# Kernel tuning notes

Measured on AMD Instinct MI355X. Metric: run time of the kernel, lower is better.

The kernel has to match this reference:

```python
import jax, jax.numpy as jnp
import numpy as np


def _lstm_cell(x, h, c, Wih, Whh, b):
    # torch LSTM gate order: i, f, g, o
    g = x @ Wih.T + h @ Whh.T + b
    i, f, gg, o = jnp.split(g, 4, axis=-1)
    c = jax.nn.sigmoid(f) * c + jax.nn.sigmoid(i) * jnp.tanh(gg)
    h = jax.nn.sigmoid(o) * jnp.tanh(c)
    return h, c


def _run_lstm(emb, mask, Wih, Whh, b, reverse):
    # mask-gated scan emulates pack_padded_sequence: state frozen on pad steps,
    # final (h, c) equals state at last valid token of each sequence.
    B = emb.shape[0]
    H = Whh.shape[1]
    def step(carry, inp):
        h, c = carry
        x, m = inp  # x: (B, E), m: (B, 1)
        hn, cn = _lstm_cell(x, h, c, Wih, Whh, b)
        h = m * hn + (1.0 - m) * h
        c = m * cn + (1.0 - m) * c
        return (h, c), h
    xs = (jnp.swapaxes(emb, 0, 1), jnp.swapaxes(mask, 0, 1)[..., None])
    z = jnp.zeros((B, H), emb.dtype)
    (h, c), outs = jax.lax.scan(step, (z, z), xs, reverse=reverse)
    return jnp.swapaxes(outs, 0, 1), h, c  # (B, T, H), (B, H), (B, H)


def setup_inputs() -> dict:
    key = jax.random.key(0)
    ks = iter(jax.random.split(key, 40))
    B, Te, Td, E, H, Ve, Vd = 32, 64, 32, 256, 512, 32000, 32000
    s = 0.05
    def rn(shape):
        return jax.random.normal(next(ks), shape, jnp.float32) * s
    def zz(n):
        return jnp.zeros((n,), jnp.float32)
    return {
        "enc_texts": jax.random.randint(next(ks), (B, Te), 0, Ve),
        "enc_mask": jnp.ones((B, Te), jnp.float32),
        "dec_texts": jax.random.randint(next(ks), (B, Td), 0, Vd),
        "enc_emb": rn((Ve, E)),
        "dec_emb": rn((Vd, E)),
        "Wih_f": rn((4 * H, E)), "Whh_f": rn((4 * H, H)), "b_f": zz(4 * H),
        "Wih_b": rn((4 * H, E)), "Whh_b": rn((4 * H, H)), "b_b": zz(4 * H),
        "Wih_d": rn((4 * H, E + 2 * H)), "Whh_d": rn((4 * H, H)), "b_d": zz(4 * H),
        "W_h": rn((H, 2 * H)), "b_h": zz(H),
        "W_c": rn((H, 2 * H)), "b_c": zz(H),
        "W_df": rn((2 * H, 2 * H)), "b_df": zz(2 * H),
        "W_ef": rn((2 * H, 2 * H)), "b_ef": zz(2 * H),
        "W_out": rn((Vd, 3 * H)), "b_out": zz(Vd),
    }


def reference(enc_texts, enc_mask, dec_texts, enc_emb, dec_emb,
              Wih_f, Whh_f, b_f, Wih_b, Whh_b, b_b,
              Wih_d, Whh_d, b_d, W_h, b_h, W_c, b_c,
              W_df, b_df, W_ef, b_ef, W_out, b_out):
    B = enc_texts.shape[0]
    H = Whh_d.shape[1]
    # ---- encode: bidirectional LSTM over embedded source ----
    emb = enc_emb[enc_texts]  # (B, Te, E)
    out_f, hf, cf = _run_lstm(emb, enc_mask, Wih_f, Whh_f, b_f, reverse=False)
    out_b, hb, cb = _run_lstm(emb, enc_mask, Wih_b, Whh_b, b_b, reverse=True)
    enc_output = jnp.concatenate([out_f, out_b], -1) * enc_mask[..., None]  # (B, Te, 2H)
    # ---- decode_init: project concat of directional final states ----
    dec_h = jax.nn.relu(jnp.concatenate([hf, hb], -1) @ W_h.T + b_h)  # (B, H)
    dec_c = jax.nn.relu(jnp.concatenate([cf, cb], -1) @ W_c.T + b_c)  # (B, H)
    # precompute attention keys once (enc_output_fc)
    enc_feat = enc_output @ W_ef.T + b_ef  # (B, Te, 2H)
    # teacher-forcing inputs: tokens 0..Td-2
    dec_in = dec_emb[dec_texts[:, :-1]]  # (B, Td-1, E)
    ctx0 = jnp.zeros((B, 2 * H), enc_output.dtype)

    def step(carry, x):
        h, c, ctx = carry
        xin = jnp.concatenate([x, ctx], -1)  # (B, E + 2H)
        h, c = _lstm_cell(xin, h, c, Wih_d, Whh_d, b_d)
        # dot attention: query from projected (h, c)
        df = jnp.concatenate([h, c], -1) @ W_df.T + b_df  # (B, 2H)
        scores = jnp.einsum('bd,btd->bt', df, enc_feat)
        a = jax.nn.softmax(scores, axis=-1) * enc_mask
        a = a / jnp.sum(a, axis=-1, keepdims=True)
        ctx = jnp.einsum('bt,btd->bd', a, enc_output)  # (B, 2H)
        logits = jnp.concatenate([h, ctx], -1) @ W_out.T + b_out  # (B, Vd)
        return (h, c, ctx), logits

    _, logits = jax.lax.scan(step, (dec_h, dec_c, ctx0), jnp.swapaxes(dec_in, 0, 1))
    return jnp.swapaxes(logits, 0, 1)  # (B, Td-1, Vd)
```

## Files before the change

kernel.cpp:

```cpp
#include <hip/hip_runtime.h>
#include <hip/hip_bf16.h>


typedef __attribute__((ext_vector_type(8))) short bfrag_t;
typedef __attribute__((ext_vector_type(4))) float f4_t;

static __device__ __forceinline__ float bf2f(unsigned short u) {
  union { float f; unsigned int i; } v; v.i = ((unsigned int)u) << 16; return v.f;
}
static __device__ __forceinline__ unsigned short f2bf(float f) {
  union { float f; unsigned int i; } v; v.f = f;
  unsigned int r = v.i + 0x7FFFu + ((v.i >> 16) & 1u);
  return (unsigned short)(r >> 16);
}
static __device__ __forceinline__ unsigned int pack_bf2(float lo, float hi) {
  __hip_bfloat162 h2 = __float22bfloat162_rn(make_float2(lo, hi));
  union { __hip_bfloat162 h; unsigned int u; } cv; cv.h = h2;
  return cv.u;
}
static __device__ __forceinline__ float sigm(float x) {
  return __builtin_amdgcn_rcpf(1.f + __expf(-x));
}
static __device__ __forceinline__ float ftanh(float x) {
  float e = __expf(2.f * x);
  return 1.f - 2.f * __builtin_amdgcn_rcpf(e + 1.f);
}

#define GLDS16(g, l)                                                        \
  __builtin_amdgcn_global_load_lds(                                         \
      (const __attribute__((address_space(1))) void*)(g),                   \
      (__attribute__((address_space(3))) void*)(l), 16, 0, 0)

static __device__ __forceinline__ void st_f32_coh(float* p, float v) {
  asm volatile("global_store_dword %0, %1, off sc0 sc1" :: "v"(p), "v"(v) : "memory");
}
static __device__ __forceinline__ void st_u16_coh(unsigned short* p, unsigned short x) {
  asm volatile("global_store_short %0, %1, off sc0 sc1" :: "v"(p), "v"((unsigned)x) : "memory");
}
static __device__ __forceinline__ float ld_f32_coh(const float* p) {
  float v;
  asm volatile("global_load_dword %0, %1, off sc0 sc1\n\ts_waitcnt vmcnt(0)"
               : "=v"(v) : "v"(p) : "memory");
  return v;
}

static __device__ __forceinline__ void arrive8(unsigned* base) {
  __syncthreads();
  if (threadIdx.x == 0)
    __hip_atomic_fetch_add(base + (blockIdx.x & 7) * 32, 1u,
                           __ATOMIC_RELAXED, __HIP_MEMORY_SCOPE_AGENT);
}
static __device__ __forceinline__ void wait8(unsigned* base, unsigned target) {
  if (threadIdx.x < 64) {
    unsigned sum;
    do {
      unsigned v = 0;
      if (threadIdx.x < 8)
        v = __hip_atomic_load(base + threadIdx.x * 32,
                              __ATOMIC_RELAXED, __HIP_MEMORY_SCOPE_AGENT);
      v += __shfl_xor(v, 1);
      v += __shfl_xor(v, 2);
      v += __shfl_xor(v, 4);
      sum = __shfl(v, 0);
      if (sum < target) __builtin_amdgcn_s_sleep(2);
    } while (sum < target);
  }
  __syncthreads();
}
static __device__ __forceinline__ void gbar8(unsigned* base, unsigned target) {
  arrive8(base);
  wait8(base, target);
}

__global__ __launch_bounds__(256) void gemm_bt_kernel(
    const unsigned short* __restrict__ A, int lda,
    const float* __restrict__ B, int ldb, int bcol0,
    const float* __restrict__ bias, void* __restrict__ Cv, int ldc,
    int Mvalid, int K, int Mt, int swz, int obf) {
  __shared__ unsigned short As[128 * 32];
  __shared__ unsigned short Bs[128 * 32];
  int id = blockIdx.x;
  if (swz) { int x = id & 7; id = x * ((int)gridDim.x >> 3) + (id >> 3); }
  const int mb = id % Mt, nb = id / Mt;
  const int m0 = mb * 128, n0 = nb * 128;
  const int tid = threadIdx.x;
  const int w = tid >> 6, lane = tid & 63;
  const int wr = (w >> 1) * 64, wc = (w & 1) * 64;
  const int l15 = lane & 15, l4 = lane >> 4;

  const int arow = w * 16 + (lane >> 2);
  const int acol = (lane & 3) * 8;
  const unsigned short* Ag = A + (size_t)(m0 + arow) * lda + acol;

  const int brow = tid >> 1;
  const int bcol = (tid & 1) * 16;
  const float* Bg = B + (size_t)(n0 + brow) * ldb + bcol0 + bcol;
  unsigned short* Bsw = Bs + brow * 32 + bcol;

  f4_t acc[4][4];
#pragma unroll
  for (int i = 0; i < 4; ++i)
#pragma unroll
    for (int j = 0; j < 4; ++j) {
      acc[i][j].x = 0.f; acc[i][j].y = 0.f; acc[i][j].z = 0.f; acc[i][j].w = 0.f;
    }

  for (int kt = 0; kt < K; kt += 32) {
    GLDS16(Ag + kt, As + w * 512);
    GLDS16(Ag + (size_t)64 * lda + kt, As + (4 + w) * 512);
    float4 q0 = *(const float4*)(Bg + kt);
    float4 q1 = *(const float4*)(Bg + kt + 4);
    float4 q2 = *(const float4*)(Bg + kt + 8);
    float4 q3 = *(const float4*)(Bg + kt + 12);
    union { unsigned int u[8]; uint4 q[2]; } pk;
    pk.u[0] = pack_bf2(q0.x, q0.y); pk.u[1] = pack_bf2(q0.z, q0.w);
    pk.u[2] = pack_bf2(q1.x, q1.y); pk.u[3] = pack_bf2(q1.z, q1.w);
    pk.u[4] = pack_bf2(q2.x, q2.y); pk.u[5] = pack_bf2(q2.z, q2.w);
    pk.u[6] = pack_bf2(q3.x, q3.y); pk.u[7] = pack_bf2(q3.z, q3.w);
    *(uint4*)(Bsw) = pk.q[0];
    *(uint4*)(Bsw + 8) = pk.q[1];
    __syncthreads();
    bfrag_t af[4], bfv[4];
#pragma unroll
    for (int m = 0; m < 4; ++m)
      af[m] = *(const bfrag_t*)(As + (wr + m * 16 + l15) * 32 + l4 * 8);
#pragma unroll
    for (int n = 0; n < 4; ++n)
      bfv[n] = *(const bfrag_t*)(Bs + (wc + n * 16 + l15) * 32 + l4 * 8);
#pragma unroll
    for (int m = 0; m < 4; ++m)
#pragma unroll
      for (int n = 0; n < 4; ++n)
        acc[m][n] = __builtin_amdgcn_mfma_f32_16x16x32_bf16(af[m], bfv[n], acc[m][n], 0, 0, 0);
    __syncthreads();
  }

  const int crb = l4 * 4;
  float* Cf = (float*)Cv;
  unsigned short* Ch = (unsigned short*)Cv;
#pragma unroll
  for (int m = 0; m < 4; ++m)
#pragma unroll
    for (int n = 0; n < 4; ++n)
#pragma unroll
      for (int r = 0; r < 4; ++r) {
        int gr = m0 + wr + m * 16 + crb + r;
        if (gr < Mvalid) {
          int gc = n0 + wc + n * 16 + l15;
          float v = acc[m][n][r] + (bias ? bias[gc] : 0.f);
          if (obf) Ch[(size_t)gr * ldc + gc] = f2bf(v);
          else     Cf[(size_t)gr * ldc + gc] = v;
        }
      }
}

__global__ __launch_bounds__(256) void gemm_bt16_kernel(
    const unsigned short* __restrict__ A, int lda,
    const unsigned short* __restrict__ B, int ldb,
    const float* __restrict__ bias, float* __restrict__ C, int ldc,
    int Mvalid, int K, int Mt, int swz) {
  __shared__ unsigned short As[128 * 32];
  __shared__ unsigned short Bs[128 * 32];
  int id = blockIdx.x;
  if (swz) { int x = id & 7; id = x * ((int)gridDim.x >> 3) + (id >> 3); }
  const int mb = id % Mt, nb = id / Mt;
  const int m0 = mb * 128, n0 = nb * 128;
  const int tid = threadIdx.x;
  const int w = tid >> 6, lane = tid & 63;
  const int wr = (w >> 1) * 64, wc = (w & 1) * 64;
  const int l15 = lane & 15, l4 = lane >> 4;

  const int arow = w * 16 + (lane >> 2);
  const int acol = (lane & 3) * 8;
  const unsigned short* Ag = A + (size_t)(m0 + arow) * lda + acol;
  const unsigned short* Bg = B + (size_t)(n0 + arow) * ldb + acol;

  f4_t acc[4][4];
#pragma unroll
  for (int i = 0; i < 4; ++i)
#pragma unroll
    for (int j = 0; j < 4; ++j) {
      acc[i][j].x = 0.f; acc[i][j].y = 0.f; acc[i][j].z = 0.f; acc[i][j].w = 0.f;
    }

  for (int kt = 0; kt < K; kt += 32) {
    GLDS16(Ag + kt, As + w * 512);
    GLDS16(Ag + (size_t)64 * lda + kt, As + (4 + w) * 512);
    GLDS16(Bg + kt, Bs + w * 512);
    GLDS16(Bg + (size_t)64 * ldb + kt, Bs + (4 + w) * 512);
    __syncthreads();
    bfrag_t af[4], bfv[4];
#pragma unroll
    for (int m = 0; m < 4; ++m)
      af[m] = *(const bfrag_t*)(As + (wr + m * 16 + l15) * 32 + l4 * 8);
#pragma unroll
    for (int n = 0; n < 4; ++n)
      bfv[n] = *(const bfrag_t*)(Bs + (wc + n * 16 + l15) * 32 + l4 * 8);
#pragma unroll
    for (int m = 0; m < 4; ++m)
#pragma unroll
      for (int n = 0; n < 4; ++n)
        acc[m][n] = __builtin_amdgcn_mfma_f32_16x16x32_bf16(af[m], bfv[n], acc[m][n], 0, 0, 0);
    __syncthreads();
  }

  const int crb = l4 * 4;
#pragma unroll
  for (int m = 0; m < 4; ++m)
#pragma unroll
    for (int n = 0; n < 4; ++n)
#pragma unroll
      for (int r = 0; r < 4; ++r) {
        int gr = m0 + wr + m * 16 + crb + r;
        if (gr < Mvalid) {
          int gc = n0 + wc + n * 16 + l15;
          C[(size_t)gr * ldc + gc] = acc[m][n][r] + bias[gc];
        }
      }
}

__global__ __launch_bounds__(256) void wout_bf16_kernel(
    const float* __restrict__ src, unsigned short* __restrict__ dst) {
  size_t base = (size_t)blockIdx.x * 2048 + threadIdx.x * 8;
  float4 a = *(const float4*)(src + base);
  float4 b = *(const float4*)(src + base + 4);
  uint4 o;
  o.x = pack_bf2(a.x, a.y); o.y = pack_bf2(a.z, a.w);
  o.z = pack_bf2(b.x, b.y); o.w = pack_bf2(b.z, b.w);
  *(uint4*)(dst + base) = o;
}

__global__ void gather_enc_kernel(const int* __restrict__ texts,
                                  const float* __restrict__ table,
                                  unsigned short* __restrict__ out) {
  const int row = blockIdx.x;
  const int tok = texts[row];
  const float4 v = *(const float4*)(table + (size_t)tok * 256 + threadIdx.x * 4);
  unsigned short* o = out + (size_t)row * 256 + threadIdx.x * 4;
  o[0] = f2bf(v.x); o[1] = f2bf(v.y); o[2] = f2bf(v.z); o[3] = f2bf(v.w);
}

__global__ void gather_dec_kernel(const int* __restrict__ texts,
                                  const float* __restrict__ table,
                                  unsigned short* __restrict__ out) {
  const int row = blockIdx.x;
  unsigned short* o = out + (size_t)row * 256 + threadIdx.x * 4;
  if (row >= 992) { o[0] = 0; o[1] = 0; o[2] = 0; o[3] = 0; return; }
  const int b = row / 31, t2 = row - b * 31;
  const int tok = texts[b * 32 + t2];
  const float4 v = *(const float4*)(table + (size_t)tok * 256 + threadIdx.x * 4);
  o[0] = f2bf(v.x); o[1] = f2bf(v.y); o[2] = f2bf(v.z); o[3] = f2bf(v.w);
}

__global__ __launch_bounds__(256) void wdf_t_kernel(
    const float* __restrict__ W_df, const float* __restrict__ b_df,
    float* __restrict__ WT) {
  const int bid = blockIdx.x;
  if (bid < 1024) {
    __shared__ float tl[32][33];
    const int tx = (bid & 31) * 32, ty = (bid >> 5) * 32;
    const int r = threadIdx.x >> 5, c = threadIdx.x & 31;
#pragma unroll
    for (int i = 0; i < 4; ++i)
      tl[r + i * 8][c] = W_df[(size_t)(ty + r + i * 8) * 1024 + tx + c];
    __syncthreads();
#pragma unroll
    for (int i = 0; i < 4; ++i)
      WT[(size_t)(tx + r + i * 8) * 1024 + ty + c] = tl[c][r + i * 8];
  } else {
    for (int i = threadIdx.x; i < 1024; i += 256)
      WT[(size_t)1024 * 1024 + i] = b_df[i];
  }
}

__global__ __launch_bounds__(256) void mega_enc_kernel(
    const float* __restrict__ XF, const float* __restrict__ XB,
    const float* __restrict__ Whh_f, const float* __restrict__ Whh_b,
    const float* __restrict__ mask,
    unsigned short* __restrict__ HBF,
    unsigned short* __restrict__ ENCO, float* __restrict__ HFIN,
    unsigned* bar) {
  const int bi = blockIdx.x;
  const int dir = bi >> 6;
  const int u0 = (bi & 63) * 8;
  const int tid = threadIdx.x;
  const float* X = dir ? XB : XF;
  const float* W = dir ? Whh_b : Whh_f;
  unsigned short* Hbf = HBF + dir * 32768;
  unsigned* cnt = bar + dir * 256;

  __shared__ unsigned short WA[32 * 520];
  __shared__ unsigned short HB[32 * 520];
  __shared__ float Gl[32][33];

#pragma unroll
  for (int i = 0; i < 16; ++i) {
    int idx = tid + i * 256;
    int r = idx >> 7, c4 = idx & 127;
    const float4 v = *(const float4*)(W + (size_t)((r >> 3) * 512 + u0 + (r & 7)) * 512 + c4 * 4);
    *(uint2*)(WA + r * 520 + c4 * 4) = make_uint2(pack_bf2(v.x, v.y), pack_bf2(v.z, v.w));
  }
  __syncthreads();

  const int w = tid >> 6, lane = tid & 63;
  const int l15 = lane & 15, l4 = lane >> 4;
  const int wrow = (w >> 1) * 16, wcol = (w & 1) * 16;

  bfrag_t afr[16];
#pragma unroll
  for (int kk = 0; kk < 16; ++kk)
    afr[kk] = *(const bfrag_t*)(WA + (wrow + l15) * 520 + kk * 32 + l4 * 8);

  const int ob = tid & 31, ouo = tid >> 5;
  const int ou = u0 + ouo;
  float h_reg = 0.f, c_reg = 0.f;

  unsigned tgt = 0;
  for (int s = 0; s < 64; ++s) {
    const int t = dir ? (63 - s) : s;
    const int pp = s & 1;
    const float* xp = X + ((size_t)ob * 64 + t) * 2048 + ou;
    float xg0 = xp[0], xg1 = xp[512], xg2 = xp[1024], xg3 = xp[1536];
    float mval = mask[ob * 64 + t];
    const unsigned short* hsrc = Hbf + pp * 16384;
    uint4 tmp[8];
#pragma unroll
    for (int i = 0; i < 8; ++i) {
      int idx = tid + i * 256;
      int r = idx >> 6, c = idx & 63;
      asm volatile("global_load_dwordx4 %0, %1, off sc0 sc1"
                   : "=v"(tmp[i]) : "v"(hsrc + r * 512 + c * 8));
    }
    asm volatile("s_waitcnt vmcnt(0)" ::: "memory");
#pragma unroll
    for (int i = 0; i < 8; ++i) {
      int idx = tid + i * 256;
      int r = idx >> 6, c = idx & 63;
      *(uint4*)(HB + r * 520 + c * 8) = tmp[i];
    }
    __syncthreads();
    {
      f4_t ae = {0.f, 0.f, 0.f, 0.f}, ao = {0.f, 0.f, 0.f, 0.f};
#pragma unroll
      for (int kk = 0; kk < 16; kk += 2) {
        bfrag_t b0 = *(const bfrag_t*)(HB + (wcol + l15) * 520 + kk * 32 + l4 * 8);
        bfrag_t b1 = *(const bfrag_t*)(HB + (wcol + l15) * 520 + (kk + 1) * 32 + l4 * 8);
        ae = __builtin_amdgcn_mfma_f32_16x16x32_bf16(afr[kk], b0, ae, 0, 0, 0);
        ao = __builtin_amdgcn_mfma_f32_16x16x32_bf16(afr[kk + 1], b1, ao, 0, 0, 0);
      }
#pragma unroll
      for (int r = 0; r < 4; ++r)
        Gl[wrow + l4 * 4 + r][wcol + l15] = ae[r] + ao[r];
    }
    __syncthreads();
    {
      float gi = Gl[ouo][ob] + xg0;
      float gf = Gl[8 + ouo][ob] + xg1;
      float gg = Gl[16 + ouo][ob] + xg2;
      float go = Gl[24 + ouo][ob] + xg3;
      float cn = sigm(gf) * c_reg + sigm(gi) * ftanh(gg);
      float hn = sigm(go) * ftanh(cn);
      float hmix = mval * hn + (1.f - mval) * h_reg;
      float cmix = mval * cn + (1.f - mval) * c_reg;
      h_reg = hmix; c_reg = cmix;
      ENCO[((size_t)ob * 64 + t) * 1024 + dir * 512 + ou] = f2bf(hmix * mval);
      st_u16_coh(Hbf + (pp ^ 1) * 16384 + ob * 512 + ou, f2bf(hmix));
      if (s == 63) {
        HFIN[dir * 16384 + ob * 512 + ou] = hmix;
        HFIN[(2 + dir) * 16384 + ob * 512 + ou] = cmix;
      }
    }
    if (s < 63) { tgt += 64; gbar8(cnt, tgt); }
  }
}

__global__ __launch_bounds__(256) void mega_dec_kernel(
    const float* __restrict__ HFIN, const float* __restrict__ W_h,
    const float* __restrict__ b_h, const float* __restrict__ W_c,
    const float* __restrict__ b_c, const float* __restrict__ XD,
    const float* __restrict__ Wih_d, const float* __restrict__ Whh_d,
    const unsigned short* __restrict__ EFG, const unsigned short* __restrict__ ENCO,
    const float* __restrict__ mask, float* __restrict__ DECH,
    float* __restrict__ DECC, unsigned short* __restrict__ PRE0,
    unsigned short* __restrict__ ACAT, unsigned* bar) {
  const int bi = blockIdx.x;
  const int tid = threadIdx.x;
  const bool is_attn = (bi >= 128);
  const int u0 = bi * 4;
  unsigned* barB1 = bar;
  unsigned* barB2 = bar + 256;

  __shared__ union {
    struct {
      unsigned short wga[16 * 1544];
      unsigned short xb[32 * 1544];
      float gl[16][33];
    } s;
    struct {
      unsigned short efg[64 * 1160];
      float hcl[1024];
      float scl[64];
      float al[64];
    } a;
    struct { float xl[32][132]; float wi[8][132]; } ini;
  } U;

  const int ob = tid & 31, ouo = (tid >> 5) & 3, ou = u0 + ouo;
  const int w = tid >> 6, lane = tid & 63;
  const int l15 = lane & 15, l4 = lane >> 4;

  if (!is_attn) {
    {
      const int mat = bi >> 6, j0i = (bi & 63) * 8;
      const int jj = tid >> 5, b = tid & 31;
      const int sr = tid >> 5, sc = (tid & 31) * 4;
      const float* Wm = mat ? W_c : W_h;
      const float* bias = mat ? b_c : b_h;
      const float* x0 = HFIN + (size_t)(mat ? 2 : 0) * 16384;
      const float* x1 = HFIN + (size_t)(mat ? 3 : 1) * 16384;
      float acc = 0.f;
      for (int kc = 0; kc < 1024; kc += 128) {
#pragma unroll
        for (int i = 0; i < 4; ++i) {
          int r = sr + i * 8;
          const float* src = (kc < 512) ? (x0 + r * 512 + kc + sc)
                                        : (x1 + r * 512 + (kc - 512) + sc);
          *(float4*)&U.ini.xl[r][sc] = *(const float4*)src;
        }
        *(float4*)&U.ini.wi[sr][sc] = *(const float4*)(Wm + (size_t)(j0i + sr) * 1024 + kc + sc);
        __syncthreads();
#pragma unroll
        for (int k = 0; k < 128; k += 4) {
          float4 wv = *(const float4*)&U.ini.wi[jj][k];
          float4 xv = *(const float4*)&U.ini.xl[b][k];
          acc += wv.x * xv.x + wv.y * xv.y + wv.z * xv.z + wv.w * xv.w;
        }
        __syncthreads();
      }
      float v = fmaxf(acc + bias[j0i + jj], 0.f);
      if (mat == 0) {
        st_f32_coh(DECH + b * 512 + j0i + jj, v);
        st_u16_coh(PRE0 + (size_t)b * 1536 + j0i + jj, f2bf(v));
      } else {
        st_f32_coh(DECC + b * 512 + j0i + jj, v);
      }
    }
    arrive8(barB1);
    wait8(barB1, 128);

#pragma unroll
    for (int i = 0; i < 24; ++i) {
      int idx = tid + i * 256;
      int r = idx / 384, c4 = idx - (idx / 384) * 384;
      int wrow = (r >> 2) * 512 + u0 + (r & 3);
      int c = c4 * 4;
      float4 v;
      if (c < 512) v = *(const float4*)(Whh_d + (size_t)wrow * 512 + c);
      else         v = *(const float4*)(Wih_d + (size_t)wrow * 1280 + 256 + (c - 512));
      *(uint2*)(U.s.wga + r * 1544 + c) = make_uint2(pack_bf2(v.x, v.y), pack_bf2(v.z, v.w));
    }
    float h_reg = 0.f, c_reg = 0.f;
    if (tid < 128) {
      h_reg = ld_f32_coh(DECH + ob * 512 + ou);
      c_reg = ld_f32_coh(DECC + ob * 512 + ou);
    }

    f4_t cae = {0.f, 0.f, 0.f, 0.f}, cao = {0.f, 0.f, 0.f, 0.f};

    for (int t = 0; t < 31; ++t) {
      float xg0 = 0, xg1 = 0, xg2 = 0, xg3 = 0;
      if (tid < 128) {
        const float* xp = XD + ((size_t)ob * 31 + t) * 2048 + ou;
        xg0 = xp[0]; xg1 = xp[512]; xg2 = xp[1024]; xg3 = xp[1536];
      }
      if (t == 0) {
        uint4 tmp[24];
#pragma unroll
        for (int i = 0; i < 24; ++i) {
          int idx = tid + i * 256;
          int r = idx / 192, c16 = idx - (idx / 192) * 192;
          asm volatile("global_load_dwordx4 %0, %1, off sc0 sc1"
                       : "=v"(tmp[i]) : "v"(PRE0 + (size_t)r * 1536 + c16 * 8));
        }
        asm volatile("s_waitcnt vmcnt(0)" ::: "memory");
#pragma unroll
        for (int i = 0; i < 24; ++i) {
          int idx = tid + i * 256;
          int r = idx / 192, c16 = idx - (idx / 192) * 192;
          *(uint4*)(U.s.xb + r * 1544 + c16 * 8) = tmp[i];
        }
        __syncthreads();
        if (w < 2) {
          f4_t ae = {0.f, 0.f, 0.f, 0.f}, ao = {0.f, 0.f, 0.f, 0.f};
#pragma unroll
          for (int kk = 0; kk < 48; kk += 2) {
            bfrag_t a0 = *(const bfrag_t*)(U.s.wga + l15 * 1544 + kk * 32 + l4 * 8);
            bfrag_t b0 = *(const bfrag_t*)(U.s.xb + (w * 16 + l15) * 1544 + kk * 32 + l4 * 8);
            bfrag_t a1 = *(const bfrag_t*)(U.s.wga + l15 * 1544 + (kk + 1) * 32 + l4 * 8);
            bfrag_t b1 = *(const bfrag_t*)(U.s.xb + (w * 16 + l15) * 1544 + (kk + 1) * 32 + l4 * 8);
            ae = __builtin_amdgcn_mfma_f32_16x16x32_bf16(a0, b0, ae, 0, 0, 0);
            ao = __builtin_amdgcn_mfma_f32_16x16x32_bf16(a1, b1, ao, 0, 0, 0);
          }
#pragma unroll
          for (int r = 0; r < 4; ++r)
            U.s.gl[l4 * 4 + r][w * 16 + l15] = ae[r] + ao[r];
        }
      } else {
        wait8(barB2, 32u * t);
        uint4 tmp[16];
#pragma unroll
        for (int i = 0; i < 16; ++i) {
          int idx = tid + i * 256;
          int r = idx >> 7, c16 = 64 + (idx & 127);
          asm volatile("global_load_dwordx4 %0, %1, off sc0 sc1"
                       : "=v"(tmp[i]) : "v"(ACAT + ((size_t)r * 31 + (t - 1)) * 1536 + c16 * 8));
        }
        asm volatile("s_waitcnt vmcnt(8)" ::: "memory");
#pragma unroll
        for (int i = 0; i < 8; ++i) {
          int idx = tid + i * 256;
          int r = idx >> 7, c16 = 64 + (idx & 127);
          *(uint4*)(U.s.xb + r * 1544 + c16 * 8) = tmp[i];
        }
        asm volatile("s_waitcnt vmcnt(0)" ::: "memory");
#pragma unroll
        for (int i = 8; i < 16; ++i) {
          int idx = tid + i * 256;
          int r = idx >> 7, c16 = 64 + (idx & 127);
          *(uint4*)(U.s.xb + r * 1544 + c16 * 8) = tmp[i];
        }
        __syncthreads();
        if (w < 2) {
          f4_t ae = cae, ao = cao;
#pragma unroll
          for (int kk = 16; kk < 48; kk += 2) {
            bfrag_t a0 = *(const bfrag_t*)(U.s.wga + l15 * 1544 + kk * 32 + l4 * 8);
            bfrag_t b0 = *(const bfrag_t*)(U.s.xb + (w * 16 + l15) * 1544 + kk * 32 + l4 * 8);
            bfrag_t a1 = *(const bfrag_t*)(U.s.wga + l15 * 1544 + (kk + 1) * 32 + l4 * 8);
            bfrag_t b1 = *(const bfrag_t*)(U.s.xb + (w * 16 + l15) * 1544 + (kk + 1) * 32 + l4 * 8);
            ae = __builtin_amdgcn_mfma_f32_16x16x32_bf16(a0, b0, ae, 0, 0, 0);
            ao = __builtin_amdgcn_mfma_f32_16x16x32_bf16(a1, b1, ao, 0, 0, 0);
          }
#pragma unroll
          for (int r = 0; r < 4; ++r)
            U.s.gl[l4 * 4 + r][w * 16 + l15] = ae[r] + ao[r];
        }
      }
      __syncthreads();
      if (tid < 128) {
        float gi = U.s.gl[ouo][ob] + xg0;
        float gf = U.s.gl[4 + ouo][ob] + xg1;
        float gg = U.s.gl[8 + ouo][ob] + xg2;
        float go = U.s.gl[12 + ouo][ob] + xg3;
        float cn = sigm(gf) * c_reg + sigm(gi) * ftanh(gg);
        float hn = sigm(go) * ftanh(cn);
        h_reg = hn; c_reg = cn;
        st_f32_coh(DECH + ob * 512 + ou, hn);
        st_f32_coh(DECC + ob * 512 + ou, cn);
        st_u16_coh(ACAT + ((size_t)ob * 31 + t) * 1536 + ou, f2bf(hn));
      }
      arrive8(barB1);
      if (t < 30) {
        wait8(barB1, 128u * (t + 2));
        uint4 pre[8];
#pragma unroll
        for (int i = 0; i < 8; ++i) {
          int idx = tid + i * 256;
          int r = idx >> 6, c16 = idx & 63;
          asm volatile("global_load_dwordx4 %0, %1, off sc0 sc1"
                       : "=v"(pre[i]) : "v"(ACAT + ((size_t)r * 31 + t) * 1536 + c16 * 8));
        }
        asm volatile("s_waitcnt vmcnt(0)" ::: "memory");
#pragma unroll
        for (int i = 0; i < 8; ++i) {
          int idx = tid + i * 256;
          int r = idx >> 6, c16 = idx & 63;
          *(uint4*)(U.s.xb + r * 1544 + c16 * 8) = pre[i];
        }
        __syncthreads();
        if (w < 2) {
          f4_t ae = {0.f, 0.f, 0.f, 0.f}, ao = {0.f, 0.f, 0.f, 0.f};
#pragma unroll
          for (int kk = 0; kk < 16; kk += 2) {
            bfrag_t a0 = *(const bfrag_t*)(U.s.wga + l15 * 1544 + kk * 32 + l4 * 8);
            bfrag_t b0 = *(const bfrag_t*)(U.s.xb + (w * 16 + l15) * 1544 + kk * 32 + l4 * 8);
            bfrag_t a1 = *(const bfrag_t*)(U.s.wga + l15 * 1544 + (kk + 1) * 32 + l4 * 8);
            bfrag_t b1 = *(const bfrag_t*)(U.s.xb + (w * 16 + l15) * 1544 + (kk + 1) * 32 + l4 * 8);
            ae = __builtin_amdgcn_mfma_f32_16x16x32_bf16(a0, b0, ae, 0, 0, 0);
            ao = __builtin_amdgcn_mfma_f32_16x16x32_bf16(a1, b1, ao, 0, 0, 0);
          }
          cae = ae; cao = ao;
        }
      }
    }
  } else {
    const int b = bi - 128;
    for (int idx = tid; idx < 64 * 144; idx += 256) {
      int s = idx / 144, c16 = idx - (idx / 144) * 144;
      *(uint4*)(U.a.efg + s * 1160 + c16 * 8) =
          *(const uint4*)(EFG + ((size_t)b * 64 + s) * 1152 + c16 * 8);
    }
    for (int t = 0; t < 31; ++t) {
      wait8(barB1, 128u * (t + 2));
      {
        int c = tid * 4;
        const float* hp = (c < 512) ? (DECH + b * 512 + c) : (DECC + b * 512 + (c - 512));
        uint4 hv;
        asm volatile("global_load_dwordx4 %0, %1, off sc0 sc1\n\ts_waitcnt vmcnt(0)"
                     : "=v"(hv) : "v"(hp) : "memory");
        *(uint4*)&U.a.hcl[c] = hv;
      }
      __syncthreads();
      {
        const int sidx = tid >> 2, part = tid & 3;
        const unsigned short* eg = U.a.efg + sidx * 1160 + part * 256;
        const float* d = &U.a.hcl[part * 256];
        float acc = 0.f;
#pragma unroll 8
        for (int k = 0; k < 256; k += 8) {
          uint4 v = *(const uint4*)(eg + k);
          acc += bf2f((unsigned short)(v.x & 0xFFFFu)) * d[k + 0];
          acc += bf2f((unsigned short)(v.x >> 16))     * d[k + 1];
          acc += bf2f((unsigned short)(v.y & 0xFFFFu)) * d[k + 2];
          acc += bf2f((unsigned short)(v.y >> 16))     * d[k + 3];
          acc += bf2f((unsigned short)(v.z & 0xFFFFu)) * d[k + 4];
          acc += bf2f((unsigned short)(v.z >> 16))     * d[k + 5];
          acc += bf2f((unsigned short)(v.w & 0xFFFFu)) * d[k + 6];
          acc += bf2f((unsigned short)(v.w >> 16))     * d[k + 7];
        }
        acc += __shfl_xor(acc, 1);
        acc += __shfl_xor(acc, 2);
        if (part == 0)
          U.a.scl[sidx] = acc + bf2f(U.a.efg[sidx * 1160 + 1024]);
      }
      __syncthreads();
      if (tid < 64) {
        float v = U.a.scl[tid];
        float mx = v;
#pragma unroll
        for (int o = 32; o >= 1; o >>= 1) mx = fmaxf(mx, __shfl_xor(mx, o));
        float e = __expf(v - mx) * mask[b * 64 + tid];
        float sm = e;
#pragma unroll
        for (int o = 32; o >= 1; o >>= 1) sm += __shfl_xor(sm, o);
        U.a.al[tid] = e / sm;
      }
      __syncthreads();
      float c0 = 0.f, c1 = 0.f, c2 = 0.f, c3 = 0.f;
#pragma unroll 8
      for (int tp = 0; tp < 64; ++tp) {
        float a = U.a.al[tp];
        const unsigned short* eo = ENCO + ((size_t)b * 64 + tp) * 1024 + tid;
        c0 += a * bf2f(eo[0]);
        c1 += a * bf2f(eo[256]);
        c2 += a * bf2f(eo[512]);
        c3 += a * bf2f(eo[768]);
      }
      unsigned short* ap = ACAT + ((size_t)b * 31 + t) * 1536 + 512;
      st_u16_coh(ap + tid, f2bf(c0));
      st_u16_coh(ap + tid + 256, f2bf(c1));
      st_u16_coh(ap + tid + 512, f2bf(c2));
      st_u16_coh(ap + tid + 768, f2bf(c3));
      arrive8(barB2);
    }
  }
}

extern "C" void kernel_launch(void* const* d_in, const int* in_sizes, int n_in,
                              void* d_out, int out_size, void* d_ws, size_t ws_size,
                              hipStream_t stream) {
  const int*   enc_texts = (const int*)  d_in[0];
  const float* enc_mask  = (const float*)d_in[1];
  const int*   dec_texts = (const int*)  d_in[2];
  const float* enc_emb   = (const float*)d_in[3];
  const float* dec_emb   = (const float*)d_in[4];
  const float* Wih_f = (const float*)d_in[5];
  const float* Whh_f = (const float*)d_in[6];
  const float* b_f   = (const float*)d_in[7];
  const float* Wih_b = (const float*)d_in[8];
  const float* Whh_b = (const float*)d_in[9];
  const float* b_b   = (const float*)d_in[10];
  const float* Wih_d = (const float*)d_in[11];
  const float* Whh_d = (const float*)d_in[12];
  const float* b_d   = (const float*)d_in[13];
  const float* W_h   = (const float*)d_in[14];
  const float* b_h   = (const float*)d_in[15];
  const float* W_c   = (const float*)d_in[16];
  const float* b_c   = (const float*)d_in[17];
  const float* W_df  = (const float*)d_in[18];
  const float* b_df  = (const float*)d_in[19];
  const float* W_ef  = (const float*)d_in[20];
  const float* b_ef  = (const float*)d_in[21];
  const float* W_out = (const float*)d_in[22];
  const float* b_out = (const float*)d_in[23];
  float* out = (float*)d_out;

  char* ws = (char*)d_ws;
  size_t off = 0;
  auto alloc = [&](size_t bytes) {
    char* p = ws + off;
    off += (bytes + 255) & ~(size_t)255;
    return p;
  };
  unsigned short* HBF  = (unsigned short*)alloc((size_t)2 * 2 * 16384 * 2);
  float* DECH = (float*)alloc((size_t)16384 * 4);
  float* DECC = (float*)alloc((size_t)16384 * 4);
  unsigned short* PRE0 = (unsigned short*)alloc((size_t)32 * 1536 * 2);
  unsigned short* ACAT = (unsigned short*)alloc((size_t)1024 * 1536 * 2);
  unsigned* bar = (unsigned*)alloc(4096);
  unsigned* barD = bar + 512;
  size_t zbytes = off;
  float* XF = (float*)alloc((size_t)2048 * 2048 * 4);
  float* XB = (float*)alloc((size_t)2048 * 2048 * 4);
  float* XD = (float*)alloc((size_t)1024 * 2048 * 4);
  unsigned short* EFb  = (unsigned short*)alloc((size_t)2048 * 1024 * 2);
  unsigned short* ENCO = (unsigned short*)alloc((size_t)2048 * 1024 * 2);
  unsigned short* EMBB = (unsigned short*)alloc((size_t)2048 * 256 * 2);
  unsigned short* DEMB = (unsigned short*)alloc((size_t)1024 * 256 * 2);
  float* HFIN = (float*)alloc((size_t)4 * 16384 * 4);
  unsigned short* EFG = (unsigned short*)XF;
  float* WT  = XB;
  unsigned short* WOB = (unsigned short*)alloc((size_t)32000 * 1536 * 2);
  const bool use16 = (off <= ws_size);

  hipMemsetAsync(d_ws, 0, zbytes, stream);

  gather_enc_kernel<<<2048, 64, 0, stream>>>(enc_texts, enc_emb, EMBB);
  gather_dec_kernel<<<1024, 64, 0, stream>>>(dec_texts, dec_emb, DEMB);
  if (use16)
    wout_bf16_kernel<<<24000, 256, 0, stream>>>(W_out, WOB);

  dim3 blk(256);
  gemm_bt_kernel<<<256, blk, 0, stream>>>(EMBB, 256, Wih_f, 256, 0, b_f, XF, 2048, 2048, 256, 16, 0, 0);
  gemm_bt_kernel<<<256, blk, 0, stream>>>(EMBB, 256, Wih_b, 256, 0, b_b, XB, 2048, 2048, 256, 16, 0, 0);
  gemm_bt_kernel<<<128, blk, 0, stream>>>(DEMB, 256, Wih_d, 1280, 0, b_d, XD, 2048, 1024, 256, 8, 0, 0);

  mega_enc_kernel<<<128, blk, 0, stream>>>(XF, XB, Whh_f, Whh_b, enc_mask, HBF, ENCO, HFIN, bar);

  wdf_t_kernel<<<1025, blk, 0, stream>>>(W_df, b_df, WT);
  gemm_bt_kernel<<<128, blk, 0, stream>>>(ENCO, 1024, W_ef, 1024, 0, b_ef, EFb, 1024, 2048, 1024, 16, 0, 1);
  gemm_bt_kernel<<<144, blk, 0, stream>>>(EFb, 1024, WT, 1024, 0, nullptr, EFG, 1152, 2048, 1024, 16, 0, 1);

  mega_dec_kernel<<<160, blk, 0, stream>>>(HFIN, W_h, b_h, W_c, b_c, XD, Wih_d, Whh_d,
                                           EFG, ENCO, enc_mask, DECH, DECC, PRE0, ACAT, barD);

  if (use16)
    gemm_bt16_kernel<<<2000, blk, 0, stream>>>(ACAT, 1536, WOB, 1536, b_out, out, 32000, 992, 1536, 8, 1);
  else
    gemm_bt_kernel<<<2000, blk, 0, stream>>>(ACAT, 1536, W_out, 1536, 0, b_out, out, 32000, 992, 1536, 8, 1, 0);
}
```

Measured before the change: 1.237 ms.

## Overlap weight conversion and W_df transpose with recurrent LSTM kernels

The standalone W_df transpose is folded into the encoder recurrent kernel as extra idle blocks, and the W_out fp32-to-bf16 conversion is folded into the decoder kernel as 64 extra blocks. Both conversions now run on otherwise unused CUs while the latency-bound recurrences execute. The encoder recurrence is also restructured to use 64 blocks of 16 units each instead of 128 blocks of 8, so fewer blocks take part in each grid barrier. The cost is a larger per-block weight footprint and more work per block, and WT gets its own buffer because it can no longer alias XB while XB is still being read. Memory traffic from the side work may contend with the latency-sensitive recurrent steps.

```diff
diff --git a/kernel.cpp b/kernel.cpp
--- a/kernel.cpp
+++ b/kernel.cpp
@@ -219,17 +219,6 @@
       }
 }
 
-__global__ __launch_bounds__(256) void wout_bf16_kernel(
-    const float* __restrict__ src, unsigned short* __restrict__ dst) {
-  size_t base = (size_t)blockIdx.x * 2048 + threadIdx.x * 8;
-  float4 a = *(const float4*)(src + base);
-  float4 b = *(const float4*)(src + base + 4);
-  uint4 o;
-  o.x = pack_bf2(a.x, a.y); o.y = pack_bf2(a.z, a.w);
-  o.z = pack_bf2(b.x, b.y); o.w = pack_bf2(b.z, b.w);
-  *(uint4*)(dst + base) = o;
-}
-
 __global__ void gather_enc_kernel(const int* __restrict__ texts,
                                   const float* __restrict__ table,
                                   unsigned short* __restrict__ out) {
@@ -252,75 +241,87 @@
   o[0] = f2bf(v.x); o[1] = f2bf(v.y); o[2] = f2bf(v.z); o[3] = f2bf(v.w);
 }
 
-__global__ __launch_bounds__(256) void wdf_t_kernel(
-    const float* __restrict__ W_df, const float* __restrict__ b_df,
-    float* __restrict__ WT) {
-  const int bid = blockIdx.x;
-  if (bid < 1024) {
-    __shared__ float tl[32][33];
-    const int tx = (bid & 31) * 32, ty = (bid >> 5) * 32;
-    const int r = threadIdx.x >> 5, c = threadIdx.x & 31;
-#pragma unroll
-    for (int i = 0; i < 4; ++i)
-      tl[r + i * 8][c] = W_df[(size_t)(ty + r + i * 8) * 1024 + tx + c];
-    __syncthreads();
-#pragma unroll
-    for (int i = 0; i < 4; ++i)
-      WT[(size_t)(tx + r + i * 8) * 1024 + ty + c] = tl[c][r + i * 8];
-  } else {
-    for (int i = threadIdx.x; i < 1024; i += 256)
-      WT[(size_t)1024 * 1024 + i] = b_df[i];
-  }
-}
-
 __global__ __launch_bounds__(256) void mega_enc_kernel(
     const float* __restrict__ XF, const float* __restrict__ XB,
     const float* __restrict__ Whh_f, const float* __restrict__ Whh_b,
     const float* __restrict__ mask,
     unsigned short* __restrict__ HBF,
     unsigned short* __restrict__ ENCO, float* __restrict__ HFIN,
-    unsigned* bar) {
+    const float* __restrict__ W_df, const float* __restrict__ b_df,
+    float* __restrict__ WT, unsigned* bar) {
   const int bi = blockIdx.x;
-  const int dir = bi >> 6;
-  const int u0 = (bi & 63) * 8;
   const int tid = threadIdx.x;
+
+  __shared__ union {
+    struct {
+      unsigned short WA[64 * 520];
+      unsigned short HB[32 * 520];
+      float Gl[64][33];
+    } e;
+    struct { float tl[32][33]; } tr;
+  } S;
+
+  if (bi >= 64) {
+    for (int job = bi - 64; job < 1025; job += 160) {
+      if (job < 1024) {
+        const int tx = (job & 31) * 32, ty = (job >> 5) * 32;
+        const int r = tid >> 5, c = tid & 31;
+#pragma unroll
+        for (int i = 0; i < 4; ++i)
+          S.tr.tl[r + i * 8][c] = W_df[(size_t)(ty + r + i * 8) * 1024 + tx + c];
+        __syncthreads();
+#pragma unroll
+        for (int i = 0; i < 4; ++i)
+          WT[(size_t)(tx + r + i * 8) * 1024 + ty + c] = S.tr.tl[c][r + i * 8];
+        __syncthreads();
+      } else {
+        for (int i = tid; i < 1024; i += 256)
+          WT[(size_t)1024 * 1024 + i] = b_df[i];
+      }
+    }
+    return;
+  }
+
+  const int dir = bi >> 5;
+  const int u0 = (bi & 31) * 16;
   const float* X = dir ? XB : XF;
   const float* W = dir ? Whh_b : Whh_f;
   unsigned short* Hbf = HBF + dir * 32768;
   unsigned* cnt = bar + dir * 256;
 
-  __shared__ unsigned short WA[32 * 520];
-  __shared__ unsigned short HB[32 * 520];
-  __shared__ float Gl[32][33];
-
-#pragma unroll
-  for (int i = 0; i < 16; ++i) {
+#pragma unroll
+  for (int i = 0; i < 32; ++i) {
     int idx = tid + i * 256;
     int r = idx >> 7, c4 = idx & 127;
-    const float4 v = *(const float4*)(W + (size_t)((r >> 3) * 512 + u0 + (r & 7)) * 512 + c4 * 4);
-    *(uint2*)(WA + r * 520 + c4 * 4) = make_uint2(pack_bf2(v.x, v.y), pack_bf2(v.z, v.w));
+    const float4 v = *(const float4*)(W + (size_t)((r >> 4) * 512 + u0 + (r & 15)) * 512 + c4 * 4);
+    *(uint2*)(S.e.WA + r * 520 + c4 * 4) = make_uint2(pack_bf2(v.x, v.y), pack_bf2(v.z, v.w));
   }
   __syncthreads();
 
   const int w = tid >> 6, lane = tid & 63;
   const int l15 = lane & 15, l4 = lane >> 4;
-  const int wrow = (w >> 1) * 16, wcol = (w & 1) * 16;
+  const int wrow = w * 16;
 
   bfrag_t afr[16];
 #pragma unroll
   for (int kk = 0; kk < 16; ++kk)
-    afr[kk] = *(const bfrag_t*)(WA + (wrow + l15) * 520 + kk * 32 + l4 * 8);
+    afr[kk] = *(const bfrag_t*)(S.e.WA + (wrow + l15) * 520 + kk * 32 + l4 * 8);
 
   const int ob = tid & 31, ouo = tid >> 5;
-  const int ou = u0 + ouo;
-  float h_reg = 0.f, c_reg = 0.f;
+  float h_reg0 = 0.f, c_reg0 = 0.f, h_reg1 = 0.f, c_reg1 = 0.f;
 
   unsigned tgt = 0;
   for (int s = 0; s < 64; ++s) {
     const int t = dir ? (63 - s) : s;
     const int pp = s & 1;
-    const float* xp = X + ((size_t)ob * 64 + t) * 2048 + ou;
-    float xg0 = xp[0], xg1 = xp[512], xg2 = xp[1024], xg3 = xp[1536];
+    const float* xp = X + ((size_t)ob * 64 + t) * 2048 + u0;
+    float xg[2][4];
+#pragma unroll
+    for (int p = 0; p < 2; ++p) {
+      int ul = ouo + p * 8;
+      xg[p][0] = xp[ul]; xg[p][1] = xp[512 + ul];
+      xg[p][2] = xp[1024 + ul]; xg[p][3] = xp[1536 + ul];
+    }
     float mval = mask[ob * 64 + t];
     const unsigned short* hsrc = Hbf + pp * 16384;
     uint4 tmp[8];
@@ -336,28 +337,35 @@
     for (int i = 0; i < 8; ++i) {
       int idx = tid + i * 256;
       int r = idx >> 6, c = idx & 63;
-      *(uint4*)(HB + r * 520 + c * 8) = tmp[i];
+      *(uint4*)(S.e.HB + r * 520 + c * 8) = tmp[i];
     }
     __syncthreads();
     {
-      f4_t ae = {0.f, 0.f, 0.f, 0.f}, ao = {0.f, 0.f, 0.f, 0.f};
-#pragma unroll
-      for (int kk = 0; kk < 16; kk += 2) {
-        bfrag_t b0 = *(const bfrag_t*)(HB + (wcol + l15) * 520 + kk * 32 + l4 * 8);
-        bfrag_t b1 = *(const bfrag_t*)(HB + (wcol + l15) * 520 + (kk + 1) * 32 + l4 * 8);
-        ae = __builtin_amdgcn_mfma_f32_16x16x32_bf16(afr[kk], b0, ae, 0, 0, 0);
-        ao = __builtin_amdgcn_mfma_f32_16x16x32_bf16(afr[kk + 1], b1, ao, 0, 0, 0);
-      }
-#pragma unroll
-      for (int r = 0; r < 4; ++r)
-        Gl[wrow + l4 * 4 + r][wcol + l15] = ae[r] + ao[r];
+      f4_t a0 = {0.f, 0.f, 0.f, 0.f}, a1 = {0.f, 0.f, 0.f, 0.f};
+#pragma unroll
+      for (int kk = 0; kk < 16; ++kk) {
+        bfrag_t b0 = *(const bfrag_t*)(S.e.HB + l15 * 520 + kk * 32 + l4 * 8);
+        bfrag_t b1 = *(const bfrag_t*)(S.e.HB + (16 + l15) * 520 + kk * 32 + l4 * 8);
+        a0 = __builtin_amdgcn_mfma_f32_16x16x32_bf16(afr[kk], b0, a0, 0, 0, 0);
+        a1 = __builtin_amdgcn_mfma_f32_16x16x32_bf16(afr[kk], b1, a1, 0, 0, 0);
+      }
+#pragma unroll
+      for (int r = 0; r < 4; ++r) {
+        S.e.Gl[wrow + l4 * 4 + r][l15] = a0[r];
+        S.e.Gl[wrow + l4 * 4 + r][16 + l15] = a1[r];
+      }
     }
     __syncthreads();
-    {
-      float gi = Gl[ouo][ob] + xg0;
-      float gf = Gl[8 + ouo][ob] + xg1;
-      float gg = Gl[16 + ouo][ob] + xg2;
-      float go = Gl[24 + ouo][ob] + xg3;
+#pragma unroll
+    for (int p = 0; p < 2; ++p) {
+      const int ul = ouo + p * 8;
+      const int ou = u0 + ul;
+      float& h_reg = p ? h_reg1 : h_reg0;
+      float& c_reg = p ? c_reg1 : c_reg0;
+      float gi = S.e.Gl[ul][ob] + xg[p][0];
+      float gf = S.e.Gl[16 + ul][ob] + xg[p][1];
+      float gg = S.e.Gl[32 + ul][ob] + xg[p][2];
+      float go = S.e.Gl[48 + ul][ob] + xg[p][3];
       float cn = sigm(gf) * c_reg + sigm(gi) * ftanh(gg);
       float hn = sigm(go) * ftanh(cn);
       float hmix = mval * hn + (1.f - mval) * h_reg;
@@ -370,7 +378,7 @@
         HFIN[(2 + dir) * 16384 + ob * 512 + ou] = cmix;
       }
     }
-    if (s < 63) { tgt += 64; gbar8(cnt, tgt); }
+    if (s < 63) { tgt += 32; gbar8(cnt, tgt); }
   }
 }
 
@@ -382,9 +390,28 @@
     const unsigned short* __restrict__ EFG, const unsigned short* __restrict__ ENCO,
     const float* __restrict__ mask, float* __restrict__ DECH,
     float* __restrict__ DECC, unsigned short* __restrict__ PRE0,
-    unsigned short* __restrict__ ACAT, unsigned* bar) {
+    unsigned short* __restrict__ ACAT,
+    const float* __restrict__ W_out, unsigned short* __restrict__ WOB,
+    int do_conv, unsigned* bar) {
   const int bi = blockIdx.x;
   const int tid = threadIdx.x;
+
+  if (bi >= 160) {
+    if (do_conv) {
+      const int cb = bi - 160;
+      for (size_t base = (size_t)cb * 2048 + tid * 8;
+           base < (size_t)32000 * 1536; base += (size_t)64 * 2048) {
+        float4 a = *(const float4*)(W_out + base);
+        float4 b = *(const float4*)(W_out + base + 4);
+        uint4 o;
+        o.x = pack_bf2(a.x, a.y); o.y = pack_bf2(a.z, a.w);
+        o.z = pack_bf2(b.x, b.y); o.w = pack_bf2(b.z, b.w);
+        *(uint4*)(WOB + base) = o;
+      }
+    }
+    return;
+  }
+
   const bool is_attn = (bi >= 128);
   const int u0 = bi * 4;
   unsigned* barB1 = bar;
@@ -718,8 +745,8 @@
   unsigned short* EMBB = (unsigned short*)alloc((size_t)2048 * 256 * 2);
   unsigned short* DEMB = (unsigned short*)alloc((size_t)1024 * 256 * 2);
   float* HFIN = (float*)alloc((size_t)4 * 16384 * 4);
+  float* WT = (float*)alloc((size_t)1152 * 1024 * 4);
   unsigned short* EFG = (unsigned short*)XF;
-  float* WT  = XB;
   unsigned short* WOB = (unsigned short*)alloc((size_t)32000 * 1536 * 2);
   const bool use16 = (off <= ws_size);
 
@@ -727,22 +754,21 @@
 
   gather_enc_kernel<<<2048, 64, 0, stream>>>(enc_texts, enc_emb, EMBB);
   gather_dec_kernel<<<1024, 64, 0, stream>>>(dec_texts, dec_emb, DEMB);
-  if (use16)
-    wout_bf16_kernel<<<24000, 256, 0, stream>>>(W_out, WOB);
 
   dim3 blk(256);
   gemm_bt_kernel<<<256, blk, 0, stream>>>(EMBB, 256, Wih_f, 256, 0, b_f, XF, 2048, 2048, 256, 16, 0, 0);
   gemm_bt_kernel<<<256, blk, 0, stream>>>(EMBB, 256, Wih_b, 256, 0, b_b, XB, 2048, 2048, 256, 16, 0, 0);
   gemm_bt_kernel<<<128, blk, 0, stream>>>(DEMB, 256, Wih_d, 1280, 0, b_d, XD, 2048, 1024, 256, 8, 0, 0);
 
-  mega_enc_kernel<<<128, blk, 0, stream>>>(XF, XB, Whh_f, Whh_b, enc_mask, HBF, ENCO, HFIN, bar);
-
-  wdf_t_kernel<<<1025, blk, 0, stream>>>(W_df, b_df, WT);
+  mega_enc_kernel<<<224, blk, 0, stream>>>(XF, XB, Whh_f, Whh_b, enc_mask, HBF, ENCO, HFIN,
+                                           W_df, b_df, WT, bar);
+
   gemm_bt_kernel<<<128, blk, 0, stream>>>(ENCO, 1024, W_ef, 1024, 0, b_ef, EFb, 1024, 2048, 1024, 16, 0, 1);
   gemm_bt_kernel<<<144, blk, 0, stream>>>(EFb, 1024, WT, 1024, 0, nullptr, EFG, 1152, 2048, 1024, 16, 0, 1);
 
-  mega_dec_kernel<<<160, blk, 0, stream>>>(HFIN, W_h, b_h, W_c, b_c, XD, Wih_d, Whh_d,
-                                           EFG, ENCO, enc_mask, DECH, DECC, PRE0, ACAT, barD);
+  mega_dec_kernel<<<224, blk, 0, stream>>>(HFIN, W_h, b_h, W_c, b_c, XD, Wih_d, Whh_d,
+                                           EFG, ENCO, enc_mask, DECH, DECC, PRE0, ACAT,
+                                           W_out, WOB, use16 ? 1 : 0, barD);
 
   if (use16)
     gemm_bt16_kernel<<<2000, blk, 0, stream>>>(ACAT, 1536, WOB, 1536, b_out, out, 32000, 992, 1536, 8, 1);
```

Result: slower. 1.334 ms (+7.9%).

## Overlap W_out bf16 conversion and W_df transpose with encoder recurrence

Applied to the files above, without the earlier changes.

Launches 128 extra blocks in the encoder recurrence kernel. They do the W_df transpose and the W_out fp32-to-bf16 conversion while the 128 recurrence blocks run their latency-bound serial loop, and the separate wout_bf16 and wdf_t launches are removed. WT gets its own buffer, because the old aliasing with XB would conflict now that the recurrence still reads XB. The risk is that the side blocks compete for memory bandwidth and CUs with the latency-sensitive recurrence and its global barrier, and all 256 blocks must be co-resident for the barrier to avoid deadlock.

```diff
diff --git a/kernel.cpp b/kernel.cpp
--- a/kernel.cpp
+++ b/kernel.cpp
@@ -219,17 +219,6 @@
       }
 }
 
-__global__ __launch_bounds__(256) void wout_bf16_kernel(
-    const float* __restrict__ src, unsigned short* __restrict__ dst) {
-  size_t base = (size_t)blockIdx.x * 2048 + threadIdx.x * 8;
-  float4 a = *(const float4*)(src + base);
-  float4 b = *(const float4*)(src + base + 4);
-  uint4 o;
-  o.x = pack_bf2(a.x, a.y); o.y = pack_bf2(a.z, a.w);
-  o.z = pack_bf2(b.x, b.y); o.w = pack_bf2(b.z, b.w);
-  *(uint4*)(dst + base) = o;
-}
-
 __global__ void gather_enc_kernel(const int* __restrict__ texts,
                                   const float* __restrict__ table,
                                   unsigned short* __restrict__ out) {
@@ -252,53 +241,77 @@
   o[0] = f2bf(v.x); o[1] = f2bf(v.y); o[2] = f2bf(v.z); o[3] = f2bf(v.w);
 }
 
-__global__ __launch_bounds__(256) void wdf_t_kernel(
-    const float* __restrict__ W_df, const float* __restrict__ b_df,
-    float* __restrict__ WT) {
-  const int bid = blockIdx.x;
-  if (bid < 1024) {
-    __shared__ float tl[32][33];
-    const int tx = (bid & 31) * 32, ty = (bid >> 5) * 32;
-    const int r = threadIdx.x >> 5, c = threadIdx.x & 31;
-#pragma unroll
-    for (int i = 0; i < 4; ++i)
-      tl[r + i * 8][c] = W_df[(size_t)(ty + r + i * 8) * 1024 + tx + c];
-    __syncthreads();
-#pragma unroll
-    for (int i = 0; i < 4; ++i)
-      WT[(size_t)(tx + r + i * 8) * 1024 + ty + c] = tl[c][r + i * 8];
-  } else {
-    for (int i = threadIdx.x; i < 1024; i += 256)
-      WT[(size_t)1024 * 1024 + i] = b_df[i];
-  }
-}
-
 __global__ __launch_bounds__(256) void mega_enc_kernel(
     const float* __restrict__ XF, const float* __restrict__ XB,
     const float* __restrict__ Whh_f, const float* __restrict__ Whh_b,
     const float* __restrict__ mask,
     unsigned short* __restrict__ HBF,
     unsigned short* __restrict__ ENCO, float* __restrict__ HFIN,
-    unsigned* bar) {
+    const float* __restrict__ W_df, const float* __restrict__ b_df,
+    float* __restrict__ WT,
+    const float* __restrict__ W_out, unsigned short* __restrict__ WOB,
+    int do_conv, unsigned* bar) {
   const int bi = blockIdx.x;
+  const int tid = threadIdx.x;
+
+  __shared__ union {
+    struct {
+      unsigned short WA[16 * 520];
+      unsigned short HB[32 * 520];
+      float Gl[16][33];
+    } e;
+    struct { float tl[32][33]; } tr;
+  } S;
+
+  if (bi >= 128) {
+    const int wb = bi - 128;
+    for (int job = wb; job < 1025; job += 128) {
+      if (job < 1024) {
+        const int tx = (job & 31) * 32, ty = (job >> 5) * 32;
+        const int r = tid >> 5, c = tid & 31;
+#pragma unroll
+        for (int i = 0; i < 4; ++i)
+          S.tr.tl[r + i * 8][c] = W_df[(size_t)(ty + r + i * 8) * 1024 + tx + c];
+        __syncthreads();
+#pragma unroll
+        for (int i = 0; i < 4; ++i)
+          WT[(size_t)(tx + r + i * 8) * 1024 + ty + c] = S.tr.tl[c][r + i * 8];
+        __syncthreads();
+      } else {
+        for (int i = tid; i < 1024; i += 256)
+          WT[(size_t)1024 * 1024 + i] = b_df[i];
+      }
+    }
+    if (do_conv) {
+      for (size_t base = (size_t)wb * 2048 + tid * 8;
+           base < (size_t)32000 * 1536; base += (size_t)128 * 2048) {
+        float4 a = *(const float4*)(W_out + base);
+        float4 b = *(const float4*)(W_out + base + 4);
+        uint4 o;
+        o.x = pack_bf2(a.x, a.y); o.y = pack_bf2(a.z, a.w);
+        o.z = pack_bf2(b.x, b.y); o.w = pack_bf2(b.z, b.w);
+        *(uint4*)(WOB + base) = o;
+      }
+    }
+    return;
+  }
+
   const int dir = bi >> 6;
   const int u0 = (bi & 63) * 8;
-  const int tid = threadIdx.x;
   const float* X = dir ? XB : XF;
   const float* W = dir ? Whh_b : Whh_f;
   unsigned short* Hbf = HBF + dir * 32768;
   unsigned* cnt = bar + dir * 256;
 
-  __shared__ unsigned short WA[32 * 520];
-  __shared__ unsigned short HB[32 * 520];
-  __shared__ float Gl[32][33];
+  __shared__ unsigned short WA2[32 * 520];
+  __shared__ float Gl2[32][33];
 
 #pragma unroll
   for (int i = 0; i < 16; ++i) {
     int idx = tid + i * 256;
     int r = idx >> 7, c4 = idx & 127;
     const float4 v = *(const float4*)(W + (size_t)((r >> 3) * 512 + u0 + (r & 7)) * 512 + c4 * 4);
-    *(uint2*)(WA + r * 520 + c4 * 4) = make_uint2(pack_bf2(v.x, v.y), pack_bf2(v.z, v.w));
+    *(uint2*)(WA2 + r * 520 + c4 * 4) = make_uint2(pack_bf2(v.x, v.y), pack_bf2(v.z, v.w));
   }
   __syncthreads();
 
@@ -309,7 +322,7 @@
   bfrag_t afr[16];
 #pragma unroll
   for (int kk = 0; kk < 16; ++kk)
-    afr[kk] = *(const bfrag_t*)(WA + (wrow + l15) * 520 + kk * 32 + l4 * 8);
+    afr[kk] = *(const bfrag_t*)(WA2 + (wrow + l15) * 520 + kk * 32 + l4 * 8);
 
   const int ob = tid & 31, ouo = tid >> 5;
   const int ou = u0 + ouo;
@@ -336,28 +349,28 @@
     for (int i = 0; i < 8; ++i) {
       int idx = tid + i * 256;
       int r = idx >> 6, c = idx & 63;
-      *(uint4*)(HB + r * 520 + c * 8) = tmp[i];
+      *(uint4*)(S.e.HB + r * 520 + c * 8) = tmp[i];
     }
     __syncthreads();
     {
       f4_t ae = {0.f, 0.f, 0.f, 0.f}, ao = {0.f, 0.f, 0.f, 0.f};
 #pragma unroll
       for (int kk = 0; kk < 16; kk += 2) {
-        bfrag_t b0 = *(const bfrag_t*)(HB + (wcol + l15) * 520 + kk * 32 + l4 * 8);
-        bfrag_t b1 = *(const bfrag_t*)(HB + (wcol + l15) * 520 + (kk + 1) * 32 + l4 * 8);
+        bfrag_t b0 = *(const bfrag_t*)(S.e.HB + (wcol + l15) * 520 + kk * 32 + l4 * 8);
+        bfrag_t b1 = *(const bfrag_t*)(S.e.HB + (wcol + l15) * 520 + (kk + 1) * 32 + l4 * 8);
         ae = __builtin_amdgcn_mfma_f32_16x16x32_bf16(afr[kk], b0, ae, 0, 0, 0);
         ao = __builtin_amdgcn_mfma_f32_16x16x32_bf16(afr[kk + 1], b1, ao, 0, 0, 0);
       }
 #pragma unroll
       for (int r = 0; r < 4; ++r)
-        Gl[wrow + l4 * 4 + r][wcol + l15] = ae[r] + ao[r];
+        Gl2[wrow + l4 * 4 + r][wcol + l15] = ae[r] + ao[r];
     }
     __syncthreads();
     {
-      float gi = Gl[ouo][ob] + xg0;
-      float gf = Gl[8 + ouo][ob] + xg1;
-      float gg = Gl[16 + ouo][ob] + xg2;
-      float go = Gl[24 + ouo][ob] + xg3;
+      float gi = Gl2[ouo][ob] + xg0;
+      float gf = Gl2[8 + ouo][ob] + xg1;
+      float gg = Gl2[16 + ouo][ob] + xg2;
+      float go = Gl2[24 + ouo][ob] + xg3;
       float cn = sigm(gf) * c_reg + sigm(gi) * ftanh(gg);
       float hn = sigm(go) * ftanh(cn);
       float hmix = mval * hn + (1.f - mval) * h_reg;
@@ -718,8 +731,8 @@
   unsigned short* EMBB = (unsigned short*)alloc((size_t)2048 * 256 * 2);
   unsigned short* DEMB = (unsigned short*)alloc((size_t)1024 * 256 * 2);
   float* HFIN = (float*)alloc((size_t)4 * 16384 * 4);
+  float* WT = (float*)alloc((size_t)1152 * 1024 * 4);
   unsigned short* EFG = (unsigned short*)XF;
-  float* WT  = XB;
   unsigned short* WOB = (unsigned short*)alloc((size_t)32000 * 1536 * 2);
   const bool use16 = (off <= ws_size);
 
@@ -727,17 +740,15 @@
 
   gather_enc_kernel<<<2048, 64, 0, stream>>>(enc_texts, enc_emb, EMBB);
   gather_dec_kernel<<<1024, 64, 0, stream>>>(dec_texts, dec_emb, DEMB);
-  if (use16)
-    wout_bf16_kernel<<<24000, 256, 0, stream>>>(W_out, WOB);
 
   dim3 blk(256);
   gemm_bt_kernel<<<256, blk, 0, stream>>>(EMBB, 256, Wih_f, 256, 0, b_f, XF, 2048, 2048, 256, 16, 0, 0);
   gemm_bt_kernel<<<256, blk, 0, stream>>>(EMBB, 256, Wih_b, 256, 0, b_b, XB, 2048, 2048, 256, 16, 0, 0);
   gemm_bt_kernel<<<128, blk, 0, stream>>>(DEMB, 256, Wih_d, 1280, 0, b_d, XD, 2048, 1024, 256, 8, 0, 0);
 
-  mega_enc_kernel<<<128, blk, 0, stream>>>(XF, XB, Whh_f, Whh_b, enc_mask, HBF, ENCO, HFIN, bar);
-
-  wdf_t_kernel<<<1025, blk, 0, stream>>>(W_df, b_df, WT);
+  mega_enc_kernel<<<256, blk, 0, stream>>>(XF, XB, Whh_f, Whh_b, enc_mask, HBF, ENCO, HFIN,
+                                           W_df, b_df, WT, W_out, WOB, use16 ? 1 : 0, bar);
+
   gemm_bt_kernel<<<128, blk, 0, stream>>>(ENCO, 1024, W_ef, 1024, 0, b_ef, EFb, 1024, 2048, 1024, 16, 0, 1);
   gemm_bt_kernel<<<144, blk, 0, stream>>>(EFb, 1024, WT, 1024, 0, nullptr, EFG, 1152, 2048, 1024, 16, 0, 1);
 
```

Measured after the change: 1.265 ms. 2.3% more time.
